# Kernel optimization log

Measured on AMD Instinct MI355X. Metric: run time of the kernel, lower is better.

## Reference

```python
import jax, jax.numpy as jnp
import numpy as np

PARALLISM = 128          # Subarray[0]
O_BITS = 8               # ADC_resolution
SCALE = float(2 ** O_BITS - 1)          # 255.0
MAXCURRENT = 0.02 * PARALLISM           # 2.56 ; a_scale/w_scale == 2**32-1 so guards skip them


def setup_inputs() -> dict:
    key = jax.random.key(0)
    k1, k2, k3 = jax.random.split(key, 3)
    B, K, N = 8192, 4096, 4096
    x = jax.random.normal(k1, (B, K), dtype=jnp.float32) * 0.1
    weight = jax.random.normal(k2, (N, K), dtype=jnp.float32)  # torch Linear layout [out, in]
    bias = jax.random.normal(k3, (N,), dtype=jnp.float32)
    return {"x": x, "weight": weight, "bias": bias, "layer": 1}


def _quantize_partial(x):
    # output_quantize.forward: clamp to +/-maxcurrent, scale to [−scale, scale], round (STE), rescale
    y = jnp.clip(x, -MAXCURRENT, MAXCURRENT)
    y = y / MAXCURRENT * SCALE
    y = y + jax.lax.stop_gradient(jnp.round(y) - y)  # Round.apply with straight-through grad
    return y / SCALE * MAXCURRENT


def reference(x, weight, bias, layer):
    # Hard_fc: chunked VMM along the input-feature (row) dim with per-subarray ADC quantization
    B, K = x.shape
    w = weight.T                      # [K, N]
    N = w.shape[1]
    num = K // PARALLISM              # K chosen divisible by PARALLISM (32 chunks)
    xc = x.reshape(B, num, PARALLISM).swapaxes(0, 1)       # [num, B, P]
    wc = w.reshape(num, PARALLISM, N)                       # [num, P, N]

    def step(acc, chunk):
        xi, wi = chunk                # [B, P], [P, N]
        return acc + _quantize_partial(xi @ wi), None

    acc0 = jnp.zeros((B, N), dtype=x.dtype)
    out, _ = jax.lax.scan(step, acc0, (xc, wc))
    out = out + bias
    return out.reshape(B, -1)
```

## Files before the change

kernel.cpp:

```cpp
#include <hip/hip_runtime.h>


typedef __attribute__((ext_vector_type(8))) short short8;
typedef __attribute__((ext_vector_type(8))) unsigned short ushort8;
typedef __attribute__((ext_vector_type(4))) float floatx4;

#define BM 128
#define BN 256
#define BK 64

#define AS1 __attribute__((address_space(1)))
#define AS3 __attribute__((address_space(3)))

static __device__ __forceinline__ unsigned short f2bf(float f) {
    union { float f; unsigned int u; } v; v.f = f;
    unsigned int u = v.u;
    unsigned int r = (u + 0x7fffu + ((u >> 16) & 1u)) >> 16;
    return (unsigned short)r;
}

__global__ void cast_kernel(const float* __restrict__ in,
                            unsigned short* __restrict__ out,
                            long n8, float s) {
    long i = (long)blockIdx.x * 256 + threadIdx.x;
    const long stride = (long)gridDim.x * 256;
    for (; i < n8; i += stride) {
        float4 a = ((const float4*)in)[2 * i];
        float4 b = ((const float4*)in)[2 * i + 1];
        ushort8 o;
        o[0] = f2bf(a.x * s); o[1] = f2bf(a.y * s);
        o[2] = f2bf(a.z * s); o[3] = f2bf(a.w * s);
        o[4] = f2bf(b.x * s); o[5] = f2bf(b.y * s);
        o[6] = f2bf(b.z * s); o[7] = f2bf(b.w * s);
        ((ushort8*)out)[i] = o;
    }
}

__global__ __launch_bounds__(512, 2) void vmm_kernel(
    const unsigned short* __restrict__ A,
    const unsigned short* __restrict__ Bw,
    const float* __restrict__ bias,
    float* __restrict__ out,
    int N, int K)
{
    __shared__ unsigned short sA[3 * BM * BK];
    __shared__ unsigned short sB[3 * BN * BK];

    const int tid  = threadIdx.x;
    const int wid  = tid >> 6;
    const int lane = tid & 63;

    const int ntn = N / BN;
    int mt, ntile;
    if (gridDim.x == 1024 && ntn == 16) {
        const int g   = blockIdx.x & 7;
        const int idx = blockIdx.x >> 3;
        mt    = (g << 3) + ((idx >> 2) & 7);
        ntile = ((idx >> 5) << 2) + (idx & 3);
    } else {
        mt = blockIdx.x / ntn;
        ntile = blockIdx.x - mt * ntn;
    }
    const int m0 = mt * BM;
    const int n0 = ntile * BN;

    const int waveM = (wid >> 2) * 64;
    const int waveN = (wid & 3) * 64;

    const int r0  = (wid << 3) + (lane >> 3);
    const int csw = (((lane & 7) ^ (lane >> 3)) << 3);
    const unsigned short* gA = A  + (long)(m0 + r0) * K + csw;
    const unsigned short* gB = Bw + (long)(n0 + r0) * K + csw;

    const int c0 = (((lane >> 4) ^ (lane & 7)) << 3);
    int aoff[4], boff[4];
    #pragma unroll
    for (int t = 0; t < 4; ++t) {
        aoff[t] = (waveM + t * 16 + (lane & 15)) * BK + c0;
        boff[t] = (waveN + t * 16 + (lane & 15)) * BK + c0;
    }

    floatx4 acc[4][4];
    floatx4 macc[4][4];
    #pragma unroll
    for (int i = 0; i < 4; ++i)
        #pragma unroll
        for (int j = 0; j < 4; ++j) {
            acc[i][j]  = (floatx4){0.f, 0.f, 0.f, 0.f};
            macc[i][j] = (floatx4){0.f, 0.f, 0.f, 0.f};
        }

    #define STAGE(buf, ksrc) do {                                              \
        const long ko_ = (ksrc);                                               \
        __builtin_amdgcn_global_load_lds((const AS1 void*)(gA + ko_),          \
            (AS3 void*)(sA + (buf) * 8192 + wid * 512), 16, 0, 0);             \
        __builtin_amdgcn_global_load_lds((const AS1 void*)(gA + 64 * (long)K + ko_), \
            (AS3 void*)(sA + (buf) * 8192 + 4096 + wid * 512), 16, 0, 0);      \
        __builtin_amdgcn_global_load_lds((const AS1 void*)(gB + ko_),          \
            (AS3 void*)(sB + (buf) * 16384 + wid * 512), 16, 0, 0);            \
        __builtin_amdgcn_global_load_lds((const AS1 void*)(gB + 64 * (long)K + ko_), \
            (AS3 void*)(sB + (buf) * 16384 + 4096 + wid * 512), 16, 0, 0);     \
        __builtin_amdgcn_global_load_lds((const AS1 void*)(gB + 128 * (long)K + ko_), \
            (AS3 void*)(sB + (buf) * 16384 + 8192 + wid * 512), 16, 0, 0);     \
        __builtin_amdgcn_global_load_lds((const AS1 void*)(gB + 192 * (long)K + ko_), \
            (AS3 void*)(sB + (buf) * 16384 + 12288 + wid * 512), 16, 0, 0);    \
    } while (0)

    const int NT = K / BK;
    STAGE(0, 0);
    STAGE(1, BK);

    int buf = 0;
    for (int t = 0; t < NT; ++t) {
        if (t < NT - 1)
            asm volatile("s_waitcnt vmcnt(6)\n\ts_barrier" ::: "memory");
        else
            asm volatile("s_waitcnt vmcnt(0)\n\ts_barrier" ::: "memory");

        const unsigned short* pa = sA + buf * 8192;
        const unsigned short* pb = sB + buf * 16384;
        short8 af[2][4], bfr[2][4];
        #pragma unroll
        for (int tm = 0; tm < 4; ++tm) {
            af[0][tm] = *(const short8*)(pa + aoff[tm]);
            af[1][tm] = *(const short8*)(pa + (aoff[tm] ^ 32));
        }
        #pragma unroll
        for (int tn = 0; tn < 4; ++tn) {
            bfr[0][tn] = *(const short8*)(pb + boff[tn]);
            bfr[1][tn] = *(const short8*)(pb + (boff[tn] ^ 32));
        }

        if (t + 2 < NT) {
            const int nb = (buf >= 1) ? buf - 1 : 2;
            STAGE(nb, (long)(t + 2) * BK);
        }

        __builtin_amdgcn_s_setprio(1);
        #pragma unroll
        for (int h = 0; h < 2; ++h)
            #pragma unroll
            for (int tm = 0; tm < 4; ++tm)
                #pragma unroll
                for (int tn = 0; tn < 4; ++tn)
                    acc[tm][tn] = __builtin_amdgcn_mfma_f32_16x16x32_bf16(
                        af[h][tm], bfr[h][tn], acc[tm][tn], 0, 0, 0);
        __builtin_amdgcn_s_setprio(0);

        if (t & 1) {
            #pragma unroll
            for (int tm = 0; tm < 4; ++tm)
                #pragma unroll
                for (int tn = 0; tn < 4; ++tn) {
                    #pragma unroll
                    for (int r = 0; r < 4; ++r) {
                        float v = acc[tm][tn][r];
                        v = __builtin_amdgcn_fmed3f(v, -255.0f, 255.0f);
                        v = __builtin_rintf(v);
                        macc[tm][tn][r] += v;
                    }
                    acc[tm][tn] = (floatx4){0.f, 0.f, 0.f, 0.f};
                }
        }
        buf = (buf == 2) ? 0 : buf + 1;
    }

    const float invs = 2.56f / 255.0f;
    #pragma unroll
    for (int tn = 0; tn < 4; ++tn) {
        const int col = n0 + waveN + tn * 16 + (lane & 15);
        const float bv = bias[col];
        #pragma unroll
        for (int tm = 0; tm < 4; ++tm) {
            const int row = m0 + waveM + tm * 16 + (lane >> 4) * 4;
            #pragma unroll
            for (int r = 0; r < 4; ++r)
                out[(long)(row + r) * N + col] = macc[tm][tn][r] * invs + bv;
        }
    }
    #undef STAGE
}

extern "C" void kernel_launch(void* const* d_in, const int* in_sizes, int n_in,
                              void* d_out, int out_size, void* d_ws, size_t ws_size,
                              hipStream_t stream) {
    const float* x    = (const float*)d_in[0];
    const float* w    = (const float*)d_in[1];
    const float* bias = (const float*)d_in[2];

    const int N = in_sizes[2];
    const int K = in_sizes[1] / N;
    const int B = in_sizes[0] / K;
    float* out = (float*)d_out;

    unsigned short* xb = (unsigned short*)d_ws;
    unsigned short* wb = xb + (size_t)B * K;

    cast_kernel<<<2048, 256, 0, stream>>>(x, xb, ((long)B * K) / 8, 1.0f);
    cast_kernel<<<2048, 256, 0, stream>>>(w, wb, ((long)N * K) / 8, 99.609375f);

    const int nblocks = (N / BN) * (B / BM);
    vmm_kernel<<<nblocks, 512, 0, stream>>>(xb, wb, bias, out, N, K);
}
```

Measured before the change: 593.2 us.

## Split K-tile into two half-phases interleaving LDS reads, prefetch and MFMA

Restructures the main loop so each BK=64 tile is processed in two halves. Each half loads its LDS fragments and issues part of the next-stage global-to-LDS prefetch (A plus the first B row in the first half, the remaining B rows in the second), then runs 16 MFMAs, with extra barriers keeping waves in lockstep. The quantize step for the previous pair of tiles is moved ahead of the MFMAs, and a final quantize is added after the loop. The aim is to spread memory issue and LDS reads across the compute so they overlap better with MFMA, and to lower register pressure by holding only half the fragments at once. The cost is four barriers per iteration instead of one.

After: 617.8 us. +4.1%, slower.

```diff
diff --git a/kernel.cpp b/kernel.cpp
--- a/kernel.cpp
+++ b/kernel.cpp
@@ -90,80 +90,101 @@
             macc[i][j] = (floatx4){0.f, 0.f, 0.f, 0.f};
         }
 
-    #define STAGE(buf, ksrc) do {                                              \
-        const long ko_ = (ksrc);                                               \
-        __builtin_amdgcn_global_load_lds((const AS1 void*)(gA + ko_),          \
+    #define STAGE_A(buf, ko_) do {                                             \
+        __builtin_amdgcn_global_load_lds((const AS1 void*)(gA + (ko_)),        \
             (AS3 void*)(sA + (buf) * 8192 + wid * 512), 16, 0, 0);             \
-        __builtin_amdgcn_global_load_lds((const AS1 void*)(gA + 64 * (long)K + ko_), \
+        __builtin_amdgcn_global_load_lds((const AS1 void*)(gA + 64 * (long)K + (ko_)), \
             (AS3 void*)(sA + (buf) * 8192 + 4096 + wid * 512), 16, 0, 0);      \
-        __builtin_amdgcn_global_load_lds((const AS1 void*)(gB + ko_),          \
+        __builtin_amdgcn_global_load_lds((const AS1 void*)(gB + (ko_)),        \
             (AS3 void*)(sB + (buf) * 16384 + wid * 512), 16, 0, 0);            \
-        __builtin_amdgcn_global_load_lds((const AS1 void*)(gB + 64 * (long)K + ko_), \
+    } while (0)
+    #define STAGE_B(buf, ko_) do {                                             \
+        __builtin_amdgcn_global_load_lds((const AS1 void*)(gB + 64 * (long)K + (ko_)), \
             (AS3 void*)(sB + (buf) * 16384 + 4096 + wid * 512), 16, 0, 0);     \
-        __builtin_amdgcn_global_load_lds((const AS1 void*)(gB + 128 * (long)K + ko_), \
+        __builtin_amdgcn_global_load_lds((const AS1 void*)(gB + 128 * (long)K + (ko_)), \
             (AS3 void*)(sB + (buf) * 16384 + 8192 + wid * 512), 16, 0, 0);     \
-        __builtin_amdgcn_global_load_lds((const AS1 void*)(gB + 192 * (long)K + ko_), \
+        __builtin_amdgcn_global_load_lds((const AS1 void*)(gB + 192 * (long)K + (ko_)), \
             (AS3 void*)(sB + (buf) * 16384 + 12288 + wid * 512), 16, 0, 0);    \
     } while (0)
 
     const int NT = K / BK;
-    STAGE(0, 0);
-    STAGE(1, BK);
+    STAGE_A(0, 0); STAGE_B(0, 0);
+    STAGE_A(1, BK); STAGE_B(1, BK);
+    asm volatile("s_waitcnt vmcnt(6)\n\ts_barrier" ::: "memory");
 
     int buf = 0;
     for (int t = 0; t < NT; ++t) {
-        if (t < NT - 1)
-            asm volatile("s_waitcnt vmcnt(6)\n\ts_barrier" ::: "memory");
-        else
-            asm volatile("s_waitcnt vmcnt(0)\n\ts_barrier" ::: "memory");
-
+        const int nb = (buf >= 1) ? buf - 1 : 2;
+        const long ksrc = (long)(t + 2) * BK;
+        const bool pf = (t + 2 < NT);
         const unsigned short* pa = sA + buf * 8192;
         const unsigned short* pb = sB + buf * 16384;
-        short8 af[2][4], bfr[2][4];
-        #pragma unroll
-        for (int tm = 0; tm < 4; ++tm) {
-            af[0][tm] = *(const short8*)(pa + aoff[tm]);
-            af[1][tm] = *(const short8*)(pa + (aoff[tm] ^ 32));
-        }
-        #pragma unroll
-        for (int tn = 0; tn < 4; ++tn) {
-            bfr[0][tn] = *(const short8*)(pb + boff[tn]);
-            bfr[1][tn] = *(const short8*)(pb + (boff[tn] ^ 32));
-        }
-
-        if (t + 2 < NT) {
-            const int nb = (buf >= 1) ? buf - 1 : 2;
-            STAGE(nb, (long)(t + 2) * BK);
-        }
-
-        __builtin_amdgcn_s_setprio(1);
-        #pragma unroll
-        for (int h = 0; h < 2; ++h)
-            #pragma unroll
-            for (int tm = 0; tm < 4; ++tm)
-                #pragma unroll
-                for (int tn = 0; tn < 4; ++tn)
-                    acc[tm][tn] = __builtin_amdgcn_mfma_f32_16x16x32_bf16(
-                        af[h][tm], bfr[h][tn], acc[tm][tn], 0, 0, 0);
-        __builtin_amdgcn_s_setprio(0);
-
-        if (t & 1) {
+
+        short8 a0[4], b0[4];
+        #pragma unroll
+        for (int i = 0; i < 4; ++i) a0[i] = *(const short8*)(pa + aoff[i]);
+        #pragma unroll
+        for (int i = 0; i < 4; ++i) b0[i] = *(const short8*)(pb + boff[i]);
+        if (pf) STAGE_A(nb, ksrc);
+
+        if (t && !(t & 1)) {
             #pragma unroll
             for (int tm = 0; tm < 4; ++tm)
                 #pragma unroll
                 for (int tn = 0; tn < 4; ++tn) {
                     #pragma unroll
                     for (int r = 0; r < 4; ++r) {
-                        float v = acc[tm][tn][r];
-                        v = __builtin_amdgcn_fmed3f(v, -255.0f, 255.0f);
-                        v = __builtin_rintf(v);
+                        float v = __builtin_rintf(
+                            __builtin_amdgcn_fmed3f(acc[tm][tn][r], -255.0f, 255.0f));
                         macc[tm][tn][r] += v;
                     }
                     acc[tm][tn] = (floatx4){0.f, 0.f, 0.f, 0.f};
                 }
         }
+
+        asm volatile("s_barrier" ::: "memory");
+        __builtin_amdgcn_s_setprio(1);
+        #pragma unroll
+        for (int tm = 0; tm < 4; ++tm)
+            #pragma unroll
+            for (int tn = 0; tn < 4; ++tn)
+                acc[tm][tn] = __builtin_amdgcn_mfma_f32_16x16x32_bf16(
+                    a0[tm], b0[tn], acc[tm][tn], 0, 0, 0);
+        __builtin_amdgcn_s_setprio(0);
+        asm volatile("s_barrier" ::: "memory");
+
+        short8 a1[4], b1[4];
+        #pragma unroll
+        for (int i = 0; i < 4; ++i) a1[i] = *(const short8*)(pa + (aoff[i] ^ 32));
+        #pragma unroll
+        for (int i = 0; i < 4; ++i) b1[i] = *(const short8*)(pb + (boff[i] ^ 32));
+        if (pf) STAGE_B(nb, ksrc);
+
+        asm volatile("s_barrier" ::: "memory");
+        __builtin_amdgcn_s_setprio(1);
+        #pragma unroll
+        for (int tm = 0; tm < 4; ++tm)
+            #pragma unroll
+            for (int tn = 0; tn < 4; ++tn)
+                acc[tm][tn] = __builtin_amdgcn_mfma_f32_16x16x32_bf16(
+                    a1[tm], b1[tn], acc[tm][tn], 0, 0, 0);
+        __builtin_amdgcn_s_setprio(0);
+        if (pf) asm volatile("s_waitcnt vmcnt(6)\n\ts_barrier" ::: "memory");
+        else    asm volatile("s_waitcnt vmcnt(0)\n\ts_barrier" ::: "memory");
+
         buf = (buf == 2) ? 0 : buf + 1;
     }
+
+    #pragma unroll
+    for (int tm = 0; tm < 4; ++tm)
+        #pragma unroll
+        for (int tn = 0; tn < 4; ++tn)
+            #pragma unroll
+            for (int r = 0; r < 4; ++r) {
+                float v = __builtin_rintf(
+                    __builtin_amdgcn_fmed3f(acc[tm][tn][r], -255.0f, 255.0f));
+                macc[tm][tn][r] += v;
+            }
 
     const float invs = 2.56f / 255.0f;
     #pragma unroll
@@ -178,7 +199,8 @@
                 out[(long)(row + r) * N + col] = macc[tm][tn][r] * invs + bv;
         }
     }
-    #undef STAGE
+    #undef STAGE_A
+    #undef STAGE_B
 }
 
 extern "C" void kernel_launch(void* const* d_in, const int* in_sizes, int n_in,
```
